# Kernel optimization log

Hardware: AMD Instinct MI355X
Metric: run time of the kernel (lower is better)

Reference implementation:

```python
import jax, jax.numpy as jnp
import numpy as np

# Emformer config (from torchaudio.models.Emformer in BasicNet4)
D, H, FFN, L = 512, 4, 128, 4      # input_dim, num_heads, ffn_dim, num_layers
SEG, RC = 4, 1                     # segment_length, right_context_length
B, T = 8, 1025
U = T - RC                         # utterance length = 1024
NSEG = -(-U // SEG)                # 256 segments
R = NSEG * RC                      # total right-context frames = 256
DH = D // H


def _right_context_indices():
    # torchaudio _gen_right_context: segment i's right context = frames [(i+1)*SEG : (i+1)*SEG+RC],
    # last block = input[T-RC:]
    idx = [np.arange((i + 1) * SEG, (i + 1) * SEG + RC) for i in range(NSEG - 1)]
    idx.append(np.arange(T - RC, T))
    return np.concatenate(idx)


def _attention_mask():
    # Rows / cols ordered [right-context blocks (seg order), utterance frames].
    # A query belonging to segment i may attend to segment i's right-context block
    # and segment i's utterance frames (left_context_length=0, no memory bank).
    seg_rc = np.repeat(np.arange(NSEG), RC)
    seg_u = np.arange(U) // SEG
    seg_q = np.concatenate([seg_rc, seg_u])
    seg_k = np.concatenate([seg_rc, seg_u])
    return seg_q[:, None] == seg_k[None, :]  # (R+U, R+U), True = allowed


def _ln(x, g, b, eps=1e-5):
    mu = jnp.mean(x, -1, keepdims=True)
    var = jnp.mean(jnp.square(x - mu), -1, keepdims=True)
    return (x - mu) * jax.lax.rsqrt(var + eps) * g + b


def setup_inputs() -> dict:
    key = jax.random.key(0)
    ks = jax.random.split(key, 8)
    s = 0.02
    return {
        "x": jax.random.normal(ks[0], (B, T, D), jnp.float32),
        "Wq": jax.random.normal(ks[1], (L, D, D), jnp.float32) * s,
        "bq": jnp.zeros((L, D), jnp.float32),
        "Wkv": jax.random.normal(ks[2], (L, 2 * D, D), jnp.float32) * s,
        "bkv": jnp.zeros((L, 2 * D), jnp.float32),
        "Wo": jax.random.normal(ks[3], (L, D, D), jnp.float32) * s,
        "bo": jnp.zeros((L, D), jnp.float32),
        "W1": jax.random.normal(ks[4], (L, FFN, D), jnp.float32) * s,
        "b1": jnp.zeros((L, FFN), jnp.float32),
        "W2": jax.random.normal(ks[5], (L, D, FFN), jnp.float32) * s,
        "b2": jnp.zeros((L, D), jnp.float32),
        "ln_in_g": jnp.ones((L, D), jnp.float32),
        "ln_in_b": jnp.zeros((L, D), jnp.float32),
        "ff_ln_g": jnp.ones((L, D), jnp.float32),
        "ff_ln_b": jnp.zeros((L, D), jnp.float32),
        "ln_out_g": jnp.ones((L, D), jnp.float32),
        "ln_out_b": jnp.zeros((L, D), jnp.float32),
    }


def reference(x, Wq, bq, Wkv, bkv, Wo, bo, W1, b1, W2, b2,
              ln_in_g, ln_in_b, ff_ln_g, ff_ln_b, ln_out_g, ln_out_b):
    rc_idx = jnp.asarray(_right_context_indices())
    allowed = jnp.asarray(_attention_mask())
    scale = DH ** -0.5
    u = x[:, :U]          # (B, U, D) utterance
    r = x[:, rc_idx]      # (B, R, D) gathered right-context blocks
    for l in range(L):
        cat = jnp.concatenate([r, u], axis=1)            # (B, R+U, D)
        ln = _ln(cat, ln_in_g[l], ln_in_b[l])            # pre-attention LN
        q = (ln @ Wq[l].T + bq[l]).reshape(B, R + U, H, DH)
        kv = ln @ Wkv[l].T + bkv[l]
        k = kv[..., :D].reshape(B, R + U, H, DH)
        v = kv[..., D:].reshape(B, R + U, H, DH)
        scores = jnp.einsum("bqhd,bkhd->bhqk", q * scale, k)
        scores = jnp.where(allowed, scores, -jnp.inf)
        probs = jax.nn.softmax(scores, axis=-1)
        attn = jnp.einsum("bhqk,bkhd->bqhd", probs, v).reshape(B, R + U, D)
        rc_out = attn @ Wo[l].T + bo[l] + cat            # residual w/ pre-LN input
        h = _ln(rc_out, ff_ln_g[l], ff_ln_b[l])
        h = jax.nn.relu(h @ W1[l].T + b1[l]) @ W2[l].T + b2[l]
        rc_out = _ln(rc_out + h, ln_out_g[l], ln_out_b[l])
        r, u = rc_out[:, :R], rc_out[:, R:]
    return u.mean(axis=1)  # (B, D): mean-pool over utterance frames
```

## Files before the change

kernel.cpp:

```cpp
#include <hip/hip_runtime.h>
#include <cstdint>
#include <cstddef>

#define D_    512
#define H_    4
#define DH_   128
#define FFN_  128
#define L_    4
#define B_    8
#define T_    1025
#define U_    1024
#define NSEG_ 256
#define R_    256
#define TOT_  1280
#define M_    (B_*TOT_)
#define CH_   1536

typedef __attribute__((ext_vector_type(8))) short bf16x8;
typedef __attribute__((ext_vector_type(4))) float f32x4;
typedef unsigned short u16;

__device__ __forceinline__ u16 f2bf(float f) {
  unsigned u = __builtin_bit_cast(unsigned, f);
  u += 0x7fff + ((u >> 16) & 1);
  return (u16)(u >> 16);
}
__device__ __forceinline__ float bf2f(u16 h) {
  unsigned u = ((unsigned)h) << 16;
  return __builtin_bit_cast(float, u);
}

__device__ __forceinline__ void gload_lds16(const void* g, void* l) {
  __builtin_amdgcn_global_load_lds(
      (const __attribute__((address_space(1))) unsigned*)g,
      (__attribute__((address_space(3))) unsigned*)l, 16, 0, 0);
}

__global__ __launch_bounds__(256)
void cvt_all_k(const float* __restrict__ Wq, const float* __restrict__ Wkv,
               const float* __restrict__ Wo, const float* __restrict__ W1,
               const float* __restrict__ W2, const float* __restrict__ bq,
               const float* __restrict__ bkv,
               u16* __restrict__ WQKVb, u16* __restrict__ Wob,
               u16* __restrict__ W1b, u16* __restrict__ W2b,
               float* __restrict__ bQKV) {
  int i4 = blockIdx.x * 256 + threadIdx.x;
  if (i4 < 786432) {
    int e = i4 * 4;
    int l = e / 786432;
    int rem = e - l * 786432;
    int n = rem >> 9, k = rem & 511;
    const float* src = (n < 512) ? (Wq + (size_t)l * 262144 + n * 512 + k)
                                 : (Wkv + (size_t)l * 524288 + (n - 512) * 512 + k);
    float4 v = *(const float4*)src;
    ushort4 o; o.x = f2bf(v.x); o.y = f2bf(v.y); o.z = f2bf(v.z); o.w = f2bf(v.w);
    *(ushort4*)(WQKVb + e) = o;
  } else if (i4 < 1048576) {
    int e = (i4 - 786432) * 4;
    float4 v = *(const float4*)(Wo + e);
    ushort4 o; o.x = f2bf(v.x); o.y = f2bf(v.y); o.z = f2bf(v.z); o.w = f2bf(v.w);
    *(ushort4*)(Wob + e) = o;
  } else if (i4 < 1114112) {
    int e = (i4 - 1048576) * 4;
    float4 v = *(const float4*)(W1 + e);
    ushort4 o; o.x = f2bf(v.x); o.y = f2bf(v.y); o.z = f2bf(v.z); o.w = f2bf(v.w);
    *(ushort4*)(W1b + e) = o;
  } else if (i4 < 1179648) {
    int e = (i4 - 1114112) * 4;
    float4 v = *(const float4*)(W2 + e);
    ushort4 o; o.x = f2bf(v.x); o.y = f2bf(v.y); o.z = f2bf(v.z); o.w = f2bf(v.w);
    *(ushort4*)(W2b + e) = o;
  } else if (i4 < 1181184) {
    int e = (i4 - 1179648) * 4;
    int l = e / 1536, n = e - l * 1536;
#pragma unroll
    for (int t = 0; t < 4; ++t) {
      int nn = n + t;
      bQKV[e + t] = (nn < 512) ? bq[l * 512 + nn] : bkv[l * 1024 + (nn - 512)];
    }
  }
}

__global__ __launch_bounds__(256)
void gather_ln_k(const float* __restrict__ x, const float* __restrict__ g,
                 const float* __restrict__ bb, float* __restrict__ X,
                 u16* __restrict__ LNb) {
  int row = blockIdx.x;
  int tid = threadIdx.x;
  int b = row / TOT_, p = row % TOT_;
  int t = (p < R_) ? ((p < R_ - 1) ? 4 * (p + 1) : (T_ - 1)) : (p - R_);
  const float* xr = x + ((size_t)b * T_ + t) * D_;
  float e0 = xr[tid], e1 = xr[tid + 256];
  X[(size_t)row * D_ + tid] = e0;
  X[(size_t)row * D_ + tid + 256] = e1;
  float s = e0 + e1, ss = e0 * e0 + e1 * e1;
#pragma unroll
  for (int off = 32; off > 0; off >>= 1) {
    s  += __shfl_down(s, off);
    ss += __shfl_down(ss, off);
  }
  __shared__ float red[10];
  int wid = tid >> 6, lane = tid & 63;
  if (lane == 0) { red[wid] = s; red[4 + wid] = ss; }
  __syncthreads();
  if (tid == 0) {
    float S = red[0] + red[1] + red[2] + red[3];
    float SS = red[4] + red[5] + red[6] + red[7];
    float mu = S * (1.0f / D_);
    float var = SS * (1.0f / D_) - mu * mu;
    if (var < 0.f) var = 0.f;
    red[8] = mu; red[9] = rsqrtf(var + 1e-5f);
  }
  __syncthreads();
  float mu = red[8], rs = red[9];
  u16* yr = LNb + (size_t)row * D_;
  yr[tid]       = f2bf((e0 - mu) * rs * g[tid]       + bb[tid]);
  yr[tid + 256] = f2bf((e1 - mu) * rs * g[tid + 256] + bb[tid + 256]);
}

#define GBK 32

__global__ __launch_bounds__(256)
void gemm_qkv(const u16* __restrict__ A, const u16* __restrict__ Bw,
              const float* __restrict__ bias, u16* __restrict__ Cout) {
  __shared__ __align__(16) u16 As[128 * GBK];
  __shared__ __align__(16) u16 Bs[128 * GBK];
  const int tid = threadIdx.x;
  const int wid = tid >> 6;
  const int lane = tid & 63;
  const int bid = blockIdx.x;
  const int xcd = bid & 7;
  const int t = bid >> 3;
  const int cb = t % 12;
  const int rb = xcd * 10 + t / 12;
  const int bm = rb * 128;
  const int bn = cb * 128;
  const int wr = wid >> 1, wc = wid & 1;

  const int srow = tid >> 2;
  const int skoff = (tid & 3) << 3;

  f32x4 acc[4][4] = {};

  const u16* Ag0 = A  + (size_t)(bm + srow)      * D_ + skoff;
  const u16* Ag1 = A  + (size_t)(bm + 64 + srow) * D_ + skoff;
  const u16* Bg0 = Bw + (size_t)(bn + srow)      * D_ + skoff;
  const u16* Bg1 = Bw + (size_t)(bn + 64 + srow) * D_ + skoff;
  u16* AsW0 = &As[(size_t)(wid * 16)      * GBK];
  u16* AsW1 = &As[(size_t)(64 + wid * 16) * GBK];
  u16* BsW0 = &Bs[(size_t)(wid * 16)      * GBK];
  u16* BsW1 = &Bs[(size_t)(64 + wid * 16) * GBK];

  const int lrow = lane & 15;
  const int lko  = (lane >> 4) * 16;

  for (int k0 = 0; k0 < D_; k0 += GBK) {
    __syncthreads();
    gload_lds16(Ag0 + k0, AsW0);
    gload_lds16(Ag1 + k0, AsW1);
    gload_lds16(Bg0 + k0, BsW0);
    gload_lds16(Bg1 + k0, BsW1);
    __syncthreads();

    bf16x8 afrag[4], bfrag[4];
#pragma unroll
    for (int m = 0; m < 4; ++m) {
      int row = wr * 64 + m * 16 + lrow;
      afrag[m] = *(const bf16x8*)((const char*)As + row * (GBK * 2) + lko);
    }
#pragma unroll
    for (int n = 0; n < 4; ++n) {
      int col = wc * 64 + n * 16 + lrow;
      bfrag[n] = *(const bf16x8*)((const char*)Bs + col * (GBK * 2) + lko);
    }
#pragma unroll
    for (int m = 0; m < 4; ++m)
#pragma unroll
      for (int n = 0; n < 4; ++n)
        acc[m][n] = __builtin_amdgcn_mfma_f32_16x16x32_bf16(
            afrag[m], bfrag[n], acc[m][n], 0, 0, 0);
  }

  const int lcol  = lane & 15;
  const int lrow4 = (lane >> 4) * 4;
#pragma unroll
  for (int m = 0; m < 4; ++m) {
    int rowbase = bm + wr * 64 + m * 16 + lrow4;
#pragma unroll
    for (int n = 0; n < 4; ++n) {
      int col = bn + wc * 64 + n * 16 + lcol;
      float bv = bias[col];
#pragma unroll
      for (int j = 0; j < 4; ++j) {
        int row = rowbase + j;
        Cout[(size_t)row * CH_ + col] = f2bf(acc[m][n][j] + bv);
      }
    }
  }
}

__global__ __launch_bounds__(256)
void gemm_oproj(const u16* __restrict__ A, const u16* __restrict__ Bw,
                const float* __restrict__ bias, float* __restrict__ Xio) {
  __shared__ __align__(16) u16 As[128 * GBK];
  __shared__ __align__(16) u16 Bs[128 * GBK];
  const int tid = threadIdx.x;
  const int wid = tid >> 6;
  const int lane = tid & 63;
  const int bid = blockIdx.x;
  const int xcd = bid & 7;
  const int t = bid >> 3;
  const int cb = t & 3;
  const int rb = xcd * 10 + (t >> 2);
  const int bm = rb * 128;
  const int bn = cb * 128;
  const int wr = wid >> 1, wc = wid & 1;

  const int srow = tid >> 2;
  const int skoff = (tid & 3) << 3;

  f32x4 acc[4][4] = {};

  const u16* Ag0 = A  + (size_t)(bm + srow)      * D_ + skoff;
  const u16* Ag1 = A  + (size_t)(bm + 64 + srow) * D_ + skoff;
  const u16* Bg0 = Bw + (size_t)(bn + srow)      * D_ + skoff;
  const u16* Bg1 = Bw + (size_t)(bn + 64 + srow) * D_ + skoff;
  u16* AsW0 = &As[(size_t)(wid * 16)      * GBK];
  u16* AsW1 = &As[(size_t)(64 + wid * 16) * GBK];
  u16* BsW0 = &Bs[(size_t)(wid * 16)      * GBK];
  u16* BsW1 = &Bs[(size_t)(64 + wid * 16) * GBK];

  const int lrow = lane & 15;
  const int lko  = (lane >> 4) * 16;

  for (int k0 = 0; k0 < D_; k0 += GBK) {
    __syncthreads();
    gload_lds16(Ag0 + k0, AsW0);
    gload_lds16(Ag1 + k0, AsW1);
    gload_lds16(Bg0 + k0, BsW0);
    gload_lds16(Bg1 + k0, BsW1);
    __syncthreads();

    bf16x8 afrag[4], bfrag[4];
#pragma unroll
    for (int m = 0; m < 4; ++m) {
      int row = wr * 64 + m * 16 + lrow;
      afrag[m] = *(const bf16x8*)((const char*)As + row * (GBK * 2) + lko);
    }
#pragma unroll
    for (int n = 0; n < 4; ++n) {
      int col = wc * 64 + n * 16 + lrow;
      bfrag[n] = *(const bf16x8*)((const char*)Bs + col * (GBK * 2) + lko);
    }
#pragma unroll
    for (int m = 0; m < 4; ++m)
#pragma unroll
      for (int n = 0; n < 4; ++n)
        acc[m][n] = __builtin_amdgcn_mfma_f32_16x16x32_bf16(
            afrag[m], bfrag[n], acc[m][n], 0, 0, 0);
  }

  const int lcol  = lane & 15;
  const int lrow4 = (lane >> 4) * 4;
#pragma unroll
  for (int m = 0; m < 4; ++m) {
    int rowbase = bm + wr * 64 + m * 16 + lrow4;
#pragma unroll
    for (int n = 0; n < 4; ++n) {
      int col = bn + wc * 64 + n * 16 + lcol;
      float bv = bias[col];
#pragma unroll
      for (int j = 0; j < 4; ++j) {
        size_t idx = (size_t)(rowbase + j) * D_ + col;
        Xio[idx] = acc[m][n][j] + bv + Xio[idx];
      }
    }
  }
}

__global__ __launch_bounds__(256)
void ffn1_ln(const float* __restrict__ X,
             const float* __restrict__ gff, const float* __restrict__ bff,
             const u16* __restrict__ W1, const float* __restrict__ b1,
             u16* __restrict__ Hout) {
  __shared__ __align__(16) u16 Aln[16 * 512];
  __shared__ __align__(16) u16 Bs[128 * 32];
  const int tid = threadIdx.x;
  const int wid = tid >> 6, lane = tid & 63;
  const int bm = blockIdx.x * 16;
  const int r  = tid >> 4;
  const int jj = tid & 15;

  const float* xr = X + (size_t)(bm + r) * D_ + jj * 32;
  float v[32];
  float s = 0.f, ss = 0.f;
#pragma unroll
  for (int i = 0; i < 8; ++i) {
    float4 q = *(const float4*)(xr + i * 4);
    v[i * 4 + 0] = q.x; v[i * 4 + 1] = q.y;
    v[i * 4 + 2] = q.z; v[i * 4 + 3] = q.w;
    s  += q.x + q.y + q.z + q.w;
    ss += q.x * q.x + q.y * q.y + q.z * q.z + q.w * q.w;
  }
#pragma unroll
  for (int off = 1; off < 16; off <<= 1) {
    s  += __shfl_xor(s, off);
    ss += __shfl_xor(ss, off);
  }
  float mu = s * (1.0f / D_);
  float var = ss * (1.0f / D_) - mu * mu;
  if (var < 0.f) var = 0.f;
  float rs = rsqrtf(var + 1e-5f);

  char* Ab = (char*)Aln;
#pragma unroll
  for (int i = 0; i < 8; ++i) {
    int c0 = jj * 32 + i * 4;
    float4 g4 = *(const float4*)(gff + c0);
    float4 b4 = *(const float4*)(bff + c0);
    ushort4 o;
    o.x = f2bf((v[i * 4 + 0] - mu) * rs * g4.x + b4.x);
    o.y = f2bf((v[i * 4 + 1] - mu) * rs * g4.y + b4.y);
    o.z = f2bf((v[i * 4 + 2] - mu) * rs * g4.z + b4.z);
    o.w = f2bf((v[i * 4 + 3] - mu) * rs * g4.w + b4.w);
    int byteoff = (r * 1024 + c0 * 2) ^ ((r & 7) << 4);
    *(ushort4*)(Ab + byteoff) = o;
  }
  __syncthreads();

  const int lrow = lane & 15;
  const int lko  = (lane >> 4) << 4;
  const int l4 = lane >> 2;
  const int k8 = (lane & 3) << 3;
  f32x4 acc[2] = {};

  for (int k0 = 0; k0 < D_; k0 += 32) {
    if (k0) __syncthreads();
#pragma unroll
    for (int p = 0; p < 2; ++p) {
      int rowb = wid * 32 + p * 16 + l4;
      gload_lds16(W1 + (size_t)rowb * D_ + k0 + k8,
                  (char*)Bs + (wid * 32 + p * 16) * 64);
    }
    __syncthreads();
    bf16x8 af = *(const bf16x8*)((const char*)Aln +
                  ((lrow * 1024 + k0 * 2 + lko) ^ ((lrow & 7) << 4)));
    bf16x8 bf[2];
#pragma unroll
    for (int n = 0; n < 2; ++n)
      bf[n] = *(const bf16x8*)((const char*)Bs + (wid * 32 + n * 16 + lrow) * 64 + lko);
#pragma unroll
    for (int n = 0; n < 2; ++n)
      acc[n] = __builtin_amdgcn_mfma_f32_16x16x32_bf16(af, bf[n], acc[n], 0, 0, 0);
  }

  const int lcol = lane & 15;
  const int lr4 = (lane >> 4) * 4;
#pragma unroll
  for (int n = 0; n < 2; ++n) {
    int col = wid * 32 + n * 16 + lcol;
    float bv = b1[col];
#pragma unroll
    for (int j = 0; j < 4; ++j) {
      int row = bm + lr4 + j;
      Hout[(size_t)row * FFN_ + col] = f2bf(fmaxf(acc[n][j] + bv, 0.f));
    }
  }
}

template <int MODE>
__global__ __launch_bounds__(256)
void gemm_row_ln(const u16* __restrict__ A, const u16* __restrict__ Bw,
                 const float* __restrict__ bias, const float* __restrict__ Rsd,
                 float* __restrict__ Xout,
                 const float* __restrict__ g1, const float* __restrict__ b1,
                 const float* __restrict__ g2, const float* __restrict__ b2,
                 u16* __restrict__ OutBf, int K) {
  __shared__ __align__(16) u16 As[16 * 32];
  __shared__ __align__(16) u16 Bs[512 * 32];
  __shared__ float wsum[4][16], wss[4][16], mu_s[16], rs_s[16];
  const int tid = threadIdx.x;
  const int wid = tid >> 6, lane = tid & 63;
  const int bm = blockIdx.x * 16;
  const int l4 = lane >> 2;
  const int k8 = (lane & 3) << 3;
  const int lrow = lane & 15;
  const int lko  = (lane >> 4) * 16;

  f32x4 acc[8] = {};

  const u16* Ag = A + (size_t)(bm + l4) * K + k8;

  for (int k0 = 0; k0 < K; k0 += 32) {
    __syncthreads();
    if (wid == 0)
      gload_lds16(Ag + k0, As);
#pragma unroll
    for (int p = 0; p < 8; ++p) {
      int row = wid * 128 + p * 16 + l4;
      gload_lds16(Bw + (size_t)row * K + k0 + k8,
                  (char*)Bs + (wid * 128 + p * 16) * 64);
    }
    __syncthreads();

    bf16x8 af = *(const bf16x8*)((const char*)As + lrow * 64 + lko);
    bf16x8 bf[8];
#pragma unroll
    for (int n = 0; n < 8; ++n)
      bf[n] = *(const bf16x8*)((const char*)Bs + (wid * 128 + n * 16 + lrow) * 64 + lko);
#pragma unroll
    for (int n = 0; n < 8; ++n)
      acc[n] = __builtin_amdgcn_mfma_f32_16x16x32_bf16(af, bf[n], acc[n], 0, 0, 0);
  }

  const int lcol = lane & 15;
  const int lr4 = (lane >> 4) * 4;
#pragma unroll
  for (int n = 0; n < 8; ++n) {
    int col = wid * 128 + n * 16 + lcol;
    float bv = bias[col];
#pragma unroll
    for (int j = 0; j < 4; ++j) {
      int row = bm + lr4 + j;
      float t = acc[n][j] + bv + Rsd[(size_t)row * D_ + col];
      acc[n][j] = t;
    }
  }

  {
    float s0[4] = {}, s1[4] = {};
#pragma unroll
    for (int n = 0; n < 8; ++n)
#pragma unroll
      for (int j = 0; j < 4; ++j) {
        float v = acc[n][j];
        s0[j] += v; s1[j] += v * v;
      }
#pragma unroll
    for (int off = 1; off < 16; off <<= 1)
#pragma unroll
      for (int j = 0; j < 4; ++j) {
        s0[j] += __shfl_xor(s0[j], off);
        s1[j] += __shfl_xor(s1[j], off);
      }
    if ((lane & 15) == 0) {
#pragma unroll
      for (int j = 0; j < 4; ++j) {
        wsum[wid][lr4 + j] = s0[j]; wss[wid][lr4 + j] = s1[j];
      }
    }
  }
  __syncthreads();
  if (tid < 16) {
    float S  = wsum[0][tid] + wsum[1][tid] + wsum[2][tid] + wsum[3][tid];
    float SS = wss[0][tid] + wss[1][tid] + wss[2][tid] + wss[3][tid];
    float mu = S * (1.0f / D_);
    float var = SS * (1.0f / D_) - mu * mu;
    if (var < 0.f) var = 0.f;
    mu_s[tid] = mu; rs_s[tid] = rsqrtf(var + 1e-5f);
  }
  __syncthreads();

  float gg[8], bv2[8];
#pragma unroll
  for (int n = 0; n < 8; ++n) {
    int col = wid * 128 + n * 16 + lcol;
    gg[n] = g1[col]; bv2[n] = b1[col];
  }
#pragma unroll
  for (int n = 0; n < 8; ++n) {
    int col = wid * 128 + n * 16 + lcol;
#pragma unroll
    for (int j = 0; j < 4; ++j) {
      int r = lr4 + j;
      int row = bm + r;
      float ln = (acc[n][j] - mu_s[r]) * rs_s[r] * gg[n] + bv2[n];
      Xout[(size_t)row * D_ + col] = ln;
      acc[n][j] = ln;
    }
  }

  if (MODE == 1) {
    __syncthreads();
    {
      float s0[4] = {}, s1[4] = {};
#pragma unroll
      for (int n = 0; n < 8; ++n)
#pragma unroll
        for (int j = 0; j < 4; ++j) {
          float v = acc[n][j];
          s0[j] += v; s1[j] += v * v;
        }
#pragma unroll
      for (int off = 1; off < 16; off <<= 1)
#pragma unroll
        for (int j = 0; j < 4; ++j) {
          s0[j] += __shfl_xor(s0[j], off);
          s1[j] += __shfl_xor(s1[j], off);
        }
      if ((lane & 15) == 0) {
#pragma unroll
        for (int j = 0; j < 4; ++j) {
          wsum[wid][lr4 + j] = s0[j]; wss[wid][lr4 + j] = s1[j];
        }
      }
    }
    __syncthreads();
    if (tid < 16) {
      float S  = wsum[0][tid] + wsum[1][tid] + wsum[2][tid] + wsum[3][tid];
      float SS = wss[0][tid] + wss[1][tid] + wss[2][tid] + wss[3][tid];
      float mu = S * (1.0f / D_);
      float var = SS * (1.0f / D_) - mu * mu;
      if (var < 0.f) var = 0.f;
      mu_s[tid] = mu; rs_s[tid] = rsqrtf(var + 1e-5f);
    }
    __syncthreads();
#pragma unroll
    for (int n = 0; n < 8; ++n) {
      int col = wid * 128 + n * 16 + lcol;
      gg[n] = g2[col]; bv2[n] = b2[col];
    }
#pragma unroll
    for (int n = 0; n < 8; ++n) {
      int col = wid * 128 + n * 16 + lcol;
#pragma unroll
      for (int j = 0; j < 4; ++j) {
        int r = lr4 + j;
        int row = bm + r;
        float ln = (acc[n][j] - mu_s[r]) * rs_s[r] * gg[n] + bv2[n];
        OutBf[(size_t)row * D_ + col] = f2bf(ln);
      }
    }
  }
}

#define QLD 516
__global__ __launch_bounds__(256)
void attn_k(const u16* __restrict__ QKV, u16* __restrict__ O) {
  int bs = blockIdx.x;
  int b = bs >> 8, s = bs & 255;
  __shared__ float Qs[5][QLD];
  __shared__ float Ks[5][QLD];
  __shared__ float Vs[5][QLD];
  __shared__ float P[H_][5][5];
  int tid = threadIdx.x;
  const float scale = 0.08838834764831845f;
  int rows[5];
  rows[0] = s;
#pragma unroll
  for (int i = 1; i < 5; ++i) rows[i] = R_ + 4 * s + (i - 1);
  for (int idx = tid; idx < 960; idx += 256) {
    int mtx = idx / 320;
    int rem = idx - mtx * 320;
    int i = rem >> 6, c8 = rem & 63;
    size_t base = ((size_t)b * TOT_ + rows[i]) * CH_ + mtx * 512 + c8 * 8;
    bf16x8 v = *(const bf16x8*)(QKV + base);
    float* dst = (mtx == 0) ? &Qs[i][c8 * 8] : (mtx == 1 ? &Ks[i][c8 * 8] : &Vs[i][c8 * 8]);
    if (mtx == 0) {
#pragma unroll
      for (int t = 0; t < 8; ++t) dst[t] = bf2f((u16)v[t]) * scale;
    } else {
#pragma unroll
      for (int t = 0; t < 8; ++t) dst[t] = bf2f((u16)v[t]);
    }
  }
  __syncthreads();
  int h = tid >> 6, lane = tid & 63;
  if (lane < 25) {
    int i = lane / 5, j = lane % 5;
    float sum = 0.f;
    const float* qp = &Qs[i][h * DH_];
    const float* kp = &Ks[j][h * DH_];
#pragma unroll 8
    for (int d = 0; d < DH_; ++d) sum += qp[d] * kp[d];
    P[h][i][j] = sum;
  }
  __syncthreads();
  if (lane < 5) {
    int i = lane;
    float m = P[h][i][0];
#pragma unroll
    for (int j = 1; j < 5; ++j) m = fmaxf(m, P[h][i][j]);
    float e[5], ssum = 0.f;
#pragma unroll
    for (int j = 0; j < 5; ++j) { e[j] = __expf(P[h][i][j] - m); ssum += e[j]; }
    float inv = 1.0f / ssum;
#pragma unroll
    for (int j = 0; j < 5; ++j) P[h][i][j] = e[j] * inv;
  }
  __syncthreads();
  for (int idx = lane; idx < 5 * DH_; idx += 64) {
    int i = idx >> 7, d = idx & (DH_ - 1);
    float o = 0.f;
#pragma unroll
    for (int j = 0; j < 5; ++j) o += P[h][i][j] * Vs[j][h * DH_ + d];
    O[((size_t)b * TOT_ + rows[i]) * D_ + h * DH_ + d] = f2bf(o);
  }
}

__global__ __launch_bounds__(256)
void mean_part_k(const float* __restrict__ X, float* __restrict__ part) {
  int d = blockIdx.x * 256 + threadIdx.x;
  int jc = blockIdx.y;
  int b = blockIdx.z;
  float acc = 0.f;
  const float* base = X + ((size_t)b * TOT_ + R_ + jc * 128) * D_ + d;
  for (int j = 0; j < 128; ++j) acc += base[(size_t)j * D_];
  part[((size_t)b * 8 + jc) * D_ + d] = acc;
}

__global__ __launch_bounds__(256)
void mean_final_k(const float* __restrict__ part, float* __restrict__ out) {
  int i = blockIdx.x * 256 + threadIdx.x;
  int b = i >> 9, d = i & (D_ - 1);
  float acc = 0.f;
#pragma unroll
  for (int c = 0; c < 8; ++c) acc += part[((size_t)b * 8 + c) * D_ + d];
  out[i] = acc * (1.0f / U_);
}

extern "C" void kernel_launch(void* const* d_in, const int* in_sizes, int n_in,
                              void* d_out, int out_size, void* d_ws, size_t ws_size,
                              hipStream_t stream) {
  const float* x      = (const float*)d_in[0];
  const float* Wq     = (const float*)d_in[1];
  const float* bq     = (const float*)d_in[2];
  const float* Wkv    = (const float*)d_in[3];
  const float* bkv    = (const float*)d_in[4];
  const float* Wo     = (const float*)d_in[5];
  const float* bo     = (const float*)d_in[6];
  const float* W1     = (const float*)d_in[7];
  const float* b1     = (const float*)d_in[8];
  const float* W2     = (const float*)d_in[9];
  const float* b2     = (const float*)d_in[10];
  const float* ln_in_g  = (const float*)d_in[11];
  const float* ln_in_b  = (const float*)d_in[12];
  const float* ff_ln_g  = (const float*)d_in[13];
  const float* ff_ln_b  = (const float*)d_in[14];
  const float* ln_out_g = (const float*)d_in[15];
  const float* ln_out_b = (const float*)d_in[16];
  float* out = (float*)d_out;

  char* wsb = (char*)d_ws;
  float* X     = (float*)wsb;
  u16*   LNbuf = (u16*)(wsb + 20971520);
  u16*   QKV   = (u16*)(wsb + 31457280);
  u16*   ATT   = (u16*)(wsb + 62914560);
  u16*   Hb    = (u16*)(wsb + 83886080);
  float* part  = (float*)(wsb + 86507520);
  u16*   WQKVb = (u16*)(wsb + 86638592);
  u16*   Wob   = (u16*)(wsb + 92930048);
  u16*   W1b   = (u16*)(wsb + 95027200);
  u16*   W2b   = (u16*)(wsb + 95551488);
  float* bQKV  = (float*)(wsb + 96075776);

  cvt_all_k<<<4614, 256, 0, stream>>>(Wq, Wkv, Wo, W1, W2, bq, bkv,
                                      WQKVb, Wob, W1b, W2b, bQKV);
  gather_ln_k<<<M_, 256, 0, stream>>>(x, ln_in_g, ln_in_b, X, LNbuf);

  for (int l = 0; l < L_; ++l) {
    const u16* WQKV_l = WQKVb + (size_t)l * CH_ * D_;
    const u16* Wo_l   = Wob   + (size_t)l * D_ * D_;
    const u16* W1_l   = W1b   + (size_t)l * FFN_ * D_;
    const u16* W2_l   = W2b   + (size_t)l * D_ * FFN_;
    const float* bQKV_l = bQKV + (size_t)l * CH_;
    const float* bo_l = bo + (size_t)l * D_;
    const float* b1_l = b1 + (size_t)l * FFN_;
    const float* b2_l = b2 + (size_t)l * D_;

    gemm_qkv<<<960, 256, 0, stream>>>(LNbuf, WQKV_l, bQKV_l, QKV);

    attn_k<<<B_ * NSEG_, 256, 0, stream>>>(QKV, ATT);

    gemm_oproj<<<320, 256, 0, stream>>>(ATT, Wo_l, bo_l, X);

    ffn1_ln<<<M_ / 16, 256, 0, stream>>>(
        X, ff_ln_g + l * D_, ff_ln_b + l * D_, W1_l, b1_l, Hb);

    if (l < L_ - 1) {
      gemm_row_ln<1><<<M_ / 16, 256, 0, stream>>>(
          Hb, W2_l, b2_l, X, X,
          ln_out_g + l * D_, ln_out_b + l * D_,
          ln_in_g + (l + 1) * D_, ln_in_b + (l + 1) * D_, LNbuf, FFN_);
    } else {
      gemm_row_ln<2><<<M_ / 16, 256, 0, stream>>>(
          Hb, W2_l, b2_l, X, X,
          ln_out_g + l * D_, ln_out_b + l * D_,
          nullptr, nullptr, nullptr, FFN_);
    }
  }

  mean_part_k<<<dim3(2, 8, 8), 256, 0, stream>>>(X, part);
  mean_final_k<<<(B_ * D_) / 256, 256, 0, stream>>>(part, out);
}
```

Before: 400.5 us.

## Fuse FFN first and second GEMMs into one kernel keeping hidden in LDS

```diff
diff --git a/kernel.cpp b/kernel.cpp
--- a/kernel.cpp
+++ b/kernel.cpp
@@ -278,53 +278,60 @@
   }
 }
 
-__global__ __launch_bounds__(256)
-void ffn1_ln(const float* __restrict__ X,
-             const float* __restrict__ gff, const float* __restrict__ bff,
-             const u16* __restrict__ W1, const float* __restrict__ b1,
-             u16* __restrict__ Hout) {
+template <int MODE>
+__global__ __launch_bounds__(256)
+void ffn_fused(const float* __restrict__ X,
+               const float* __restrict__ gff, const float* __restrict__ bff,
+               const u16* __restrict__ W1, const float* __restrict__ b1,
+               const u16* __restrict__ W2, const float* __restrict__ b2,
+               const float* __restrict__ g1, const float* __restrict__ b1o,
+               const float* __restrict__ g2, const float* __restrict__ b2i,
+               float* __restrict__ Xout, u16* __restrict__ OutBf) {
+  __shared__ __align__(16) u16 Bs[512 * 32];
   __shared__ __align__(16) u16 Aln[16 * 512];
-  __shared__ __align__(16) u16 Bs[128 * 32];
+  __shared__ float wsum[4][16], wss[4][16], mu_s[16], rs_s[16];
+  u16* Hs = Aln;
   const int tid = threadIdx.x;
   const int wid = tid >> 6, lane = tid & 63;
   const int bm = blockIdx.x * 16;
   const int r  = tid >> 4;
   const int jj = tid & 15;
 
-  const float* xr = X + (size_t)(bm + r) * D_ + jj * 32;
-  float v[32];
-  float s = 0.f, ss = 0.f;
-#pragma unroll
-  for (int i = 0; i < 8; ++i) {
-    float4 q = *(const float4*)(xr + i * 4);
-    v[i * 4 + 0] = q.x; v[i * 4 + 1] = q.y;
-    v[i * 4 + 2] = q.z; v[i * 4 + 3] = q.w;
-    s  += q.x + q.y + q.z + q.w;
-    ss += q.x * q.x + q.y * q.y + q.z * q.z + q.w * q.w;
-  }
-#pragma unroll
-  for (int off = 1; off < 16; off <<= 1) {
-    s  += __shfl_xor(s, off);
-    ss += __shfl_xor(ss, off);
-  }
-  float mu = s * (1.0f / D_);
-  float var = ss * (1.0f / D_) - mu * mu;
-  if (var < 0.f) var = 0.f;
-  float rs = rsqrtf(var + 1e-5f);
-
-  char* Ab = (char*)Aln;
-#pragma unroll
-  for (int i = 0; i < 8; ++i) {
-    int c0 = jj * 32 + i * 4;
-    float4 g4 = *(const float4*)(gff + c0);
-    float4 b4 = *(const float4*)(bff + c0);
-    ushort4 o;
-    o.x = f2bf((v[i * 4 + 0] - mu) * rs * g4.x + b4.x);
-    o.y = f2bf((v[i * 4 + 1] - mu) * rs * g4.y + b4.y);
-    o.z = f2bf((v[i * 4 + 2] - mu) * rs * g4.z + b4.z);
-    o.w = f2bf((v[i * 4 + 3] - mu) * rs * g4.w + b4.w);
-    int byteoff = (r * 1024 + c0 * 2) ^ ((r & 7) << 4);
-    *(ushort4*)(Ab + byteoff) = o;
+  {
+    const float* xr = X + (size_t)(bm + r) * D_ + jj * 32;
+    float v[32];
+    float s = 0.f, ss = 0.f;
+#pragma unroll
+    for (int i = 0; i < 8; ++i) {
+      float4 q = *(const float4*)(xr + i * 4);
+      v[i * 4 + 0] = q.x; v[i * 4 + 1] = q.y;
+      v[i * 4 + 2] = q.z; v[i * 4 + 3] = q.w;
+      s  += q.x + q.y + q.z + q.w;
+      ss += q.x * q.x + q.y * q.y + q.z * q.z + q.w * q.w;
+    }
+#pragma unroll
+    for (int off = 1; off < 16; off <<= 1) {
+      s  += __shfl_xor(s, off);
+      ss += __shfl_xor(ss, off);
+    }
+    float mu = s * (1.0f / D_);
+    float var = ss * (1.0f / D_) - mu * mu;
+    if (var < 0.f) var = 0.f;
+    float rs = rsqrtf(var + 1e-5f);
+    char* Ab = (char*)Aln;
+#pragma unroll
+    for (int i = 0; i < 8; ++i) {
+      int c0 = jj * 32 + i * 4;
+      float4 g4 = *(const float4*)(gff + c0);
+      float4 b4 = *(const float4*)(bff + c0);
+      ushort4 o;
+      o.x = f2bf((v[i * 4 + 0] - mu) * rs * g4.x + b4.x);
+      o.y = f2bf((v[i * 4 + 1] - mu) * rs * g4.y + b4.y);
+      o.z = f2bf((v[i * 4 + 2] - mu) * rs * g4.z + b4.z);
+      o.w = f2bf((v[i * 4 + 3] - mu) * rs * g4.w + b4.w);
+      int byteoff = (r * 1024 + c0 * 2) ^ ((r & 7) << 4);
+      *(ushort4*)(Ab + byteoff) = o;
+    }
   }
   __syncthreads();
 
@@ -332,7 +339,7 @@
   const int lko  = (lane >> 4) << 4;
   const int l4 = lane >> 2;
   const int k8 = (lane & 3) << 3;
-  f32x4 acc[2] = {};
+  f32x4 accA[2] = {};
 
   for (int k0 = 0; k0 < D_; k0 += 32) {
     if (k0) __syncthreads();
@@ -351,59 +358,39 @@
       bf[n] = *(const bf16x8*)((const char*)Bs + (wid * 32 + n * 16 + lrow) * 64 + lko);
 #pragma unroll
     for (int n = 0; n < 2; ++n)
-      acc[n] = __builtin_amdgcn_mfma_f32_16x16x32_bf16(af, bf[n], acc[n], 0, 0, 0);
+      accA[n] = __builtin_amdgcn_mfma_f32_16x16x32_bf16(af, bf[n], accA[n], 0, 0, 0);
   }
 
   const int lcol = lane & 15;
   const int lr4 = (lane >> 4) * 4;
+  __syncthreads();
+
 #pragma unroll
   for (int n = 0; n < 2; ++n) {
     int col = wid * 32 + n * 16 + lcol;
     float bv = b1[col];
 #pragma unroll
     for (int j = 0; j < 4; ++j) {
-      int row = bm + lr4 + j;
-      Hout[(size_t)row * FFN_ + col] = f2bf(fmaxf(acc[n][j] + bv, 0.f));
-    }
-  }
-}
-
-template <int MODE>
-__global__ __launch_bounds__(256)
-void gemm_row_ln(const u16* __restrict__ A, const u16* __restrict__ Bw,
-                 const float* __restrict__ bias, const float* __restrict__ Rsd,
-                 float* __restrict__ Xout,
-                 const float* __restrict__ g1, const float* __restrict__ b1,
-                 const float* __restrict__ g2, const float* __restrict__ b2,
-                 u16* __restrict__ OutBf, int K) {
-  __shared__ __align__(16) u16 As[16 * 32];
-  __shared__ __align__(16) u16 Bs[512 * 32];
-  __shared__ float wsum[4][16], wss[4][16], mu_s[16], rs_s[16];
-  const int tid = threadIdx.x;
-  const int wid = tid >> 6, lane = tid & 63;
-  const int bm = blockIdx.x * 16;
-  const int l4 = lane >> 2;
-  const int k8 = (lane & 3) << 3;
-  const int lrow = lane & 15;
-  const int lko  = (lane >> 4) * 16;
+      int rr = lr4 + j;
+      float hv = fmaxf(accA[n][j] + bv, 0.f);
+      int byteoff = (rr * 256 + col * 2) ^ ((rr & 7) << 4);
+      *(u16*)((char*)Hs + byteoff) = f2bf(hv);
+    }
+  }
 
   f32x4 acc[8] = {};
-
-  const u16* Ag = A + (size_t)(bm + l4) * K + k8;
-
-  for (int k0 = 0; k0 < K; k0 += 32) {
-    __syncthreads();
-    if (wid == 0)
-      gload_lds16(Ag + k0, As);
+  for (int k0 = 0; k0 < FFN_; k0 += 32) {
+    __syncthreads();
 #pragma unroll
     for (int p = 0; p < 8; ++p) {
       int row = wid * 128 + p * 16 + l4;
-      gload_lds16(Bw + (size_t)row * K + k0 + k8,
+      gload_lds16(W2 + (size_t)row * FFN_ + k0 + k8,
                   (char*)Bs + (wid * 128 + p * 16) * 64);
     }
     __syncthreads();
 
-    bf16x8 af = *(const bf16x8*)((const char*)As + lrow * 64 + lko);
+    bf16x8 af = *(const bf16x8*)((const char*)Hs +
+                  ((lrow * 256 + k0 * 2 + lko) ^ ((lrow & 7) << 4)));
     bf16x8 bf[8];
 #pragma unroll
     for (int n = 0; n < 8; ++n)
@@ -413,17 +400,14 @@
       acc[n] = __builtin_amdgcn_mfma_f32_16x16x32_bf16(af, bf[n], acc[n], 0, 0, 0);
   }
 
-  const int lcol = lane & 15;
-  const int lr4 = (lane >> 4) * 4;
 #pragma unroll
   for (int n = 0; n < 8; ++n) {
     int col = wid * 128 + n * 16 + lcol;
-    float bv = bias[col];
+    float bv = b2[col];
 #pragma unroll
     for (int j = 0; j < 4; ++j) {
       int row = bm + lr4 + j;
-      float t = acc[n][j] + bv + Rsd[(size_t)row * D_ + col];
-      acc[n][j] = t;
+      acc[n][j] = acc[n][j] + bv + X[(size_t)row * D_ + col];
     }
   }
 
@@ -465,16 +449,16 @@
 #pragma unroll
   for (int n = 0; n < 8; ++n) {
     int col = wid * 128 + n * 16 + lcol;
-    gg[n] = g1[col]; bv2[n] = b1[col];
+    gg[n] = g1[col]; bv2[n] = b1o[col];
   }
 #pragma unroll
   for (int n = 0; n < 8; ++n) {
     int col = wid * 128 + n * 16 + lcol;
 #pragma unroll
     for (int j = 0; j < 4; ++j) {
-      int r = lr4 + j;
-      int row = bm + r;
-      float ln = (acc[n][j] - mu_s[r]) * rs_s[r] * gg[n] + bv2[n];
+      int rr = lr4 + j;
+      int row = bm + rr;
+      float ln = (acc[n][j] - mu_s[rr]) * rs_s[rr] * gg[n] + bv2[n];
       Xout[(size_t)row * D_ + col] = ln;
       acc[n][j] = ln;
     }
@@ -518,16 +502,16 @@
 #pragma unroll
     for (int n = 0; n < 8; ++n) {
       int col = wid * 128 + n * 16 + lcol;
-      gg[n] = g2[col]; bv2[n] = b2[col];
+      gg[n] = g2[col]; bv2[n] = b2i[col];
     }
 #pragma unroll
     for (int n = 0; n < 8; ++n) {
       int col = wid * 128 + n * 16 + lcol;
 #pragma unroll
       for (int j = 0; j < 4; ++j) {
-        int r = lr4 + j;
-        int row = bm + r;
-        float ln = (acc[n][j] - mu_s[r]) * rs_s[r] * gg[n] + bv2[n];
+        int rr = lr4 + j;
+        int row = bm + rr;
+        float ln = (acc[n][j] - mu_s[rr]) * rs_s[rr] * gg[n] + bv2[n];
         OutBf[(size_t)row * D_ + col] = f2bf(ln);
       }
     }
@@ -646,7 +630,6 @@
   u16*   LNbuf = (u16*)(wsb + 20971520);
   u16*   QKV   = (u16*)(wsb + 31457280);
   u16*   ATT   = (u16*)(wsb + 62914560);
-  u16*   Hb    = (u16*)(wsb + 83886080);
   float* part  = (float*)(wsb + 86507520);
   u16*   WQKVb = (u16*)(wsb + 86638592);
   u16*   Wob   = (u16*)(wsb + 92930048);
@@ -674,19 +657,20 @@
 
     gemm_oproj<<<320, 256, 0, stream>>>(ATT, Wo_l, bo_l, X);
 
-    ffn1_ln<<<M_ / 16, 256, 0, stream>>>(
-        X, ff_ln_g + l * D_, ff_ln_b + l * D_, W1_l, b1_l, Hb);
-
     if (l < L_ - 1) {
-      gemm_row_ln<1><<<M_ / 16, 256, 0, stream>>>(
-          Hb, W2_l, b2_l, X, X,
+      ffn_fused<1><<<M_ / 16, 256, 0, stream>>>(
+          X, ff_ln_g + l * D_, ff_ln_b + l * D_,
+          W1_l, b1_l, W2_l, b2_l,
           ln_out_g + l * D_, ln_out_b + l * D_,
-          ln_in_g + (l + 1) * D_, ln_in_b + (l + 1) * D_, LNbuf, FFN_);
+          ln_in_g + (l + 1) * D_, ln_in_b + (l + 1) * D_,
+          X, LNbuf);
     } else {
-      gemm_row_ln<2><<<M_ / 16, 256, 0, stream>>>(
-          Hb, W2_l, b2_l, X, X,
+      ffn_fused<2><<<M_ / 16, 256, 0, stream>>>(
+          X, ff_ln_g + l * D_, ff_ln_b + l * D_,
+          W1_l, b1_l, W2_l, b2_l,
           ln_out_g + l * D_, ln_out_b + l * D_,
-          nullptr, nullptr, nullptr, FFN_);
+          nullptr, nullptr,
+          X, nullptr);
     }
   }
 
```

After: 388.2 us. 3.1% less time.
